# Kernel tuning notes

Measured on AMD Instinct MI355X. Metric: run time of the kernel, lower is better.

The kernel has to match this reference:

```python
import jax, jax.numpy as jnp
import numpy as np

F_DIM, H, O = 128, 256, 256
NQ, EQ = 64, 512
ND, ED = 50000, 600000

PARAM_SHAPES = [
    ("qW1", (F_DIM, H)), ("qb1", (H,)), ("qW2", (H, H)), ("qb2", (H,)),
    ("qW3", (H, H)),     ("qb3", (H,)), ("qW4", (H, O)), ("qb4", (O,)),
    ("dW1", (F_DIM, H)), ("db1", (H,)), ("dW2", (H, H)), ("db2", (H,)),
    ("dW3", (H, H)),     ("db3", (H,)), ("dW4", (H, O)), ("db4", (O,)),
    ("lW1", (2 * O, O)), ("lb1", (O,)),
    ("lW2", (O, O // 2)), ("lb2", (O // 2,)),
    ("lW3", (O // 2, 8)), ("lb3", (8,)),
]

def setup_inputs() -> dict:
    key = jax.random.key(0)
    ks = jax.random.split(key, 4 + len(PARAM_SHAPES))
    inp = {
        "query_in_feat": jax.random.normal(ks[0], (NQ, F_DIM), jnp.float32),
        "data_in_feat": jax.random.normal(ks[1], (ND, F_DIM), jnp.float32),
        "query_edge_list": jax.random.randint(ks[2], (2, EQ), 0, NQ),
        "data_edge_list": jax.random.randint(ks[3], (2, ED), 0, ND),
    }
    for i, (name, shape) in enumerate(PARAM_SHAPES):
        fan_in = shape[0] if len(shape) == 2 else 1
        inp[name] = jax.random.normal(ks[4 + i], shape, jnp.float32) * (1.0 / np.sqrt(fan_in))
    return inp

def _mlp2(x, W1, b1, W2, b2):
    return jnp.maximum(x @ W1 + b1, 0.0) @ W2 + b2

def _gin_conv(x, src, dst, W1, b1, W2, b2):
    # GINConv (eps=0): MLP(x_i + sum_{j->i} x_j); gather x[src], scatter-add at dst
    agg = jax.ops.segment_sum(x[src], dst, num_segments=x.shape[0])
    return _mlp2(x + agg, W1, b1, W2, b2)

def _gin(x, edge_index, p):
    src, dst = edge_index[0], edge_index[1]
    h = jnp.maximum(_gin_conv(x, src, dst, *p[:4]), 0.0)  # ReLU between convs
    return _gin_conv(h, src, dst, *p[4:])

def reference(query_in_feat, data_in_feat, query_edge_list, data_edge_list,
              qW1, qb1, qW2, qb2, qW3, qb3, qW4, qb4,
              dW1, db1, dW2, db2, dW3, db3, dW4, db4,
              lW1, lb1, lW2, lb2, lW3, lb3):
    qx = _gin(query_in_feat, query_edge_list, (qW1, qb1, qW2, qb2, qW3, qb3, qW4, qb4))
    dx = _gin(data_in_feat, data_edge_list, (dW1, db1, dW2, db2, dW3, db3, dW4, db4))
    # global_add_pool with batch = zeros -> single-graph sum
    qp = jnp.sum(qx, axis=0, keepdims=True)  # [1, O]
    dp = jnp.sum(dx, axis=0, keepdims=True)  # [1, O]
    h = jnp.concatenate([qp, dp], axis=1)    # [1, 2*O]
    h = jnp.maximum(h @ lW1 + lb1, 0.0)
    h = jnp.maximum(h @ lW2 + lb2, 0.0)
    h = jnp.maximum(h @ lW3 + lb3, 0.0)
    return h.reshape(1, 8)
```

## Files before the change

### kernel.cpp

```cpp
#include <hip/hip_runtime.h>
#include <hip/hip_bf16.h>


#define NQ 64
#define EQ 512
#define ND 50000
#define ED 600000
#define FDIM 128
#define HDIM 256

typedef __attribute__((ext_vector_type(8))) short short8;
typedef __attribute__((ext_vector_type(4))) float f32x4;
typedef __attribute__((ext_vector_type(2))) float floatx2;
typedef __attribute__((ext_vector_type(4))) unsigned short us4;
typedef __attribute__((ext_vector_type(2))) unsigned short us2;

__device__ __forceinline__ unsigned short f2bf(float f) {
    union { float f; unsigned u; } v; v.f = f;
    unsigned r = v.u + 0x7FFF + ((v.u >> 16) & 1);
    return (unsigned short)(r >> 16);
}
__device__ __forceinline__ float bf2f(unsigned short u) {
    union { unsigned u; float f; } v; v.u = ((unsigned)u) << 16;
    return v.f;
}


struct PackDesc {
    const float* W[8];
    unsigned short* Wp[8];
    int KT[8];
    int start[9];
};

__device__ __forceinline__ void pack_unit(const PackDesc& pd, int unit, int l) {
    int m = 0;
    while (m < 7 && unit >= pd.start[m + 1]) ++m;
    const int local = unit - pd.start[m];
    const int KT = pd.KT[m];
    const int kt = local % KT;
    const int ct = local / KT;
    const float* W = pd.W[m];
    unsigned short* Wp = pd.Wp[m];
    const int row = kt * 32 + (l >> 4) * 8;
    const int col = ct * 16 + (l & 15);
    short8 v;
#pragma unroll
    for (int j = 0; j < 8; ++j) v[j] = (short)f2bf(W[(size_t)(row + j) * 256 + col]);
    *(short8*)(Wp + (((size_t)(ct * KT + kt)) * 64 + l) * 8) = v;
}


__global__ void prepass(const float* __restrict__ xd, const float* __restrict__ xq,
                        unsigned short* __restrict__ bx, long long nd4, long long n4,
                        int cvt_b, PackDesc pd, int pack_units, int pack_b,
                        const int* __restrict__ d_dst, int* __restrict__ d_deg,
                        const int* __restrict__ q_dst, int* __restrict__ q_deg,
                        int d_eb) {
    const int b = blockIdx.x;
    const int tid = threadIdx.x;
    if (b < cvt_b) {
        long long i = (long long)b * 256 + tid;
        if (i >= n4) return;
        const float* src = (i < nd4) ? (xd + i * 4) : (xq + (i - nd4) * 4);
        float4 v = *(const float4*)src;
        us4 o;
        o[0] = f2bf(v.x); o[1] = f2bf(v.y); o[2] = f2bf(v.z); o[3] = f2bf(v.w);
        *(us4*)(bx + i * 4) = o;
    } else if (b < cvt_b + pack_b) {
        const int unit = (b - cvt_b) * 4 + (tid >> 6);
        if (unit < pack_units) pack_unit(pd, unit, tid & 63);
    } else {
        const int cb = b - cvt_b - pack_b;
        if (cb < d_eb) {
            int e = cb * 256 + tid;
            if (e < ED) atomicAdd(&d_deg[d_dst[e]], 1);
        } else {
            int e = (cb - d_eb) * 256 + tid;
            if (e < EQ) atomicAdd(&q_deg[q_dst[e]], 1);
        }
    }
}


__device__ __forceinline__ void scan1_body(const int* deg, int* rowptr, int* bsum,
                                           int n, int blk) {
    __shared__ int sh[256];
    const int t = threadIdx.x;
    const int i = blk * 256 + t;
    const int v = (i < n) ? deg[i] : 0;
    sh[t] = v;
    __syncthreads();
    for (int off = 1; off < 256; off <<= 1) {
        int x = (t >= off) ? sh[t - off] : 0;
        __syncthreads();
        sh[t] += x;
        __syncthreads();
    }
    if (i < n) rowptr[i] = sh[t] - v;
    if (t == 255) bsum[blk] = sh[255];
}

__global__ void scan_phase1_both(const int* __restrict__ d_deg, int* __restrict__ d_rowptr,
                                 int* __restrict__ d_bsum,
                                 const int* __restrict__ q_deg, int* __restrict__ q_rowptr,
                                 int* __restrict__ q_bsum, int dblocks) {
    int b = blockIdx.x;
    if (b < dblocks) scan1_body(d_deg, d_rowptr, d_bsum, ND, b);
    else             scan1_body(q_deg, q_rowptr, q_bsum, NQ, b - dblocks);
}

__device__ __forceinline__ void scan2_body(const int* bsum, int* boff, int* rowptr_n, int nb) {
    __shared__ int sh[256];
    const int t = threadIdx.x;
    const int v = (t < nb) ? bsum[t] : 0;
    sh[t] = v;
    __syncthreads();
    for (int off = 1; off < 256; off <<= 1) {
        int x = (t >= off) ? sh[t - off] : 0;
        __syncthreads();
        sh[t] += x;
        __syncthreads();
    }
    if (t < nb) boff[t] = sh[t] - v;
    if (t == 255) *rowptr_n = sh[255];
}

__global__ void scan_phase2_both(const int* __restrict__ d_bsum, int* __restrict__ d_boff,
                                 int* __restrict__ d_rowptr_n, int d_nb,
                                 const int* __restrict__ q_bsum, int* __restrict__ q_boff,
                                 int* __restrict__ q_rowptr_n, int q_nb) {
    if (blockIdx.x == 0) scan2_body(d_bsum, d_boff, d_rowptr_n, d_nb);
    else                 scan2_body(q_bsum, q_boff, q_rowptr_n, q_nb);
}

__global__ void scan_phase3_both(int* __restrict__ d_rowptr, const int* __restrict__ d_boff,
                                 int* __restrict__ d_cursor,
                                 int* __restrict__ q_rowptr, const int* __restrict__ q_boff,
                                 int* __restrict__ q_cursor, int dblocks) {
    int b = blockIdx.x;
    if (b < dblocks) {
        int i = b * 256 + threadIdx.x;
        if (i < ND) {
            int r = d_rowptr[i] + d_boff[b];
            d_rowptr[i] = r; d_cursor[i] = r;
        }
    } else {
        int i = (b - dblocks) * 256 + threadIdx.x;
        if (i < NQ) {
            int r = q_rowptr[i] + q_boff[b - dblocks];
            q_rowptr[i] = r; q_cursor[i] = r;
        }
    }
}

__global__ void fill_csr_both(const int* __restrict__ d_src, const int* __restrict__ d_dst,
                              int* __restrict__ d_cursor, int* __restrict__ d_csrsrc,
                              const int* __restrict__ q_src, const int* __restrict__ q_dst,
                              int* __restrict__ q_cursor, int* __restrict__ q_csrsrc,
                              int dblocks) {
    int b = blockIdx.x;
    if (b < dblocks) {
        int e = b * 256 + threadIdx.x;
        if (e < ED) {
            int p = atomicAdd(&d_cursor[d_dst[e]], 1);
            d_csrsrc[p] = d_src[e];
        }
    } else {
        int e = (b - dblocks) * 256 + threadIdx.x;
        if (e < EQ) {
            int p = atomicAdd(&q_cursor[q_dst[e]], 1);
            q_csrsrc[p] = q_src[e];
        }
    }
}


template <int F>
__global__ void gin_agg_dual(const unsigned short* __restrict__ xd, const int* __restrict__ rpd,
                             const int* __restrict__ csd, unsigned short* __restrict__ od,
                             const unsigned short* __restrict__ xq, const int* __restrict__ rpq,
                             const int* __restrict__ csq, unsigned short* __restrict__ oq) {
    constexpr int V = F / 64;
    const unsigned short* x; const int* rowptr; const int* csr; unsigned short* out; int node;
    if ((int)blockIdx.x < ND) { x = xd; rowptr = rpd; csr = csd; out = od; node = blockIdx.x; }
    else { x = xq; rowptr = rpq; csr = csq; out = oq; node = blockIdx.x - ND; }

    const int t = threadIdx.x;
    const int beg = rowptr[node];
    const int end = rowptr[node + 1];

    float acc[V];
    {
        const unsigned short* p = x + (size_t)node * F + t * V;
        if constexpr (V == 4) {
            us4 v = *(const us4*)p;
#pragma unroll
            for (int i = 0; i < 4; ++i) acc[i] = bf2f(v[i]);
        } else {
            us2 v = *(const us2*)p;
            acc[0] = bf2f(v[0]); acc[1] = bf2f(v[1]);
        }
    }
    int j = beg;
    for (; j + 1 < end; j += 2) {
        const unsigned short* p0 = x + (size_t)csr[j] * F + t * V;
        const unsigned short* p1 = x + (size_t)csr[j + 1] * F + t * V;
        if constexpr (V == 4) {
            us4 v0 = *(const us4*)p0;
            us4 v1 = *(const us4*)p1;
#pragma unroll
            for (int i = 0; i < 4; ++i) acc[i] += bf2f(v0[i]) + bf2f(v1[i]);
        } else {
            us2 v0 = *(const us2*)p0;
            us2 v1 = *(const us2*)p1;
            acc[0] += bf2f(v0[0]) + bf2f(v1[0]);
            acc[1] += bf2f(v0[1]) + bf2f(v1[1]);
        }
    }
    if (j < end) {
        const unsigned short* p0 = x + (size_t)csr[j] * F + t * V;
        if constexpr (V == 4) {
            us4 v0 = *(const us4*)p0;
#pragma unroll
            for (int i = 0; i < 4; ++i) acc[i] += bf2f(v0[i]);
        } else {
            us2 v0 = *(const us2*)p0;
            acc[0] += bf2f(v0[0]); acc[1] += bf2f(v0[1]);
        }
    }
    unsigned short* po = out + (size_t)node * F + t * V;
    if constexpr (V == 4) {
        us4 r;
#pragma unroll
        for (int i = 0; i < 4; ++i) r[i] = f2bf(acc[i]);
        *(us4*)po = r;
    } else {
        us2 r; r[0] = f2bf(acc[0]); r[1] = f2bf(acc[1]);
        *(us2*)po = r;
    }
}


__global__ void gin_agg_f8_256_dual(const unsigned char* __restrict__ xd,
                                    const int* __restrict__ rpd, const int* __restrict__ csd,
                                    unsigned short* __restrict__ od,
                                    const unsigned char* __restrict__ xq,
                                    const int* __restrict__ rpq, const int* __restrict__ csq,
                                    unsigned short* __restrict__ oq) {
    const unsigned char* x; const int* rowptr; const int* csr; unsigned short* out; int node;
    if ((int)blockIdx.x < ND) { x = xd; rowptr = rpd; csr = csd; out = od; node = blockIdx.x; }
    else { x = xq; rowptr = rpq; csr = csq; out = oq; node = blockIdx.x - ND; }

    const int t = threadIdx.x;
    const int beg = rowptr[node];
    const int end = rowptr[node + 1];

    float a0, a1, a2, a3;
    {
        const unsigned w = *(const unsigned*)(x + (size_t)node * 256 + t * 4);
        floatx2 lo = __builtin_amdgcn_cvt_pk_f32_fp8((int)w, false);
        floatx2 hi = __builtin_amdgcn_cvt_pk_f32_fp8((int)w, true);
        a0 = lo[0]; a1 = lo[1]; a2 = hi[0]; a3 = hi[1];
    }
    int j = beg;
    for (; j + 1 < end; j += 2) {
        const unsigned w0 = *(const unsigned*)(x + (size_t)csr[j] * 256 + t * 4);
        const unsigned w1 = *(const unsigned*)(x + (size_t)csr[j + 1] * 256 + t * 4);
        floatx2 l0 = __builtin_amdgcn_cvt_pk_f32_fp8((int)w0, false);
        floatx2 h0 = __builtin_amdgcn_cvt_pk_f32_fp8((int)w0, true);
        floatx2 l1 = __builtin_amdgcn_cvt_pk_f32_fp8((int)w1, false);
        floatx2 h1 = __builtin_amdgcn_cvt_pk_f32_fp8((int)w1, true);
        a0 += l0[0] + l1[0]; a1 += l0[1] + l1[1];
        a2 += h0[0] + h1[0]; a3 += h0[1] + h1[1];
    }
    if (j < end) {
        const unsigned w0 = *(const unsigned*)(x + (size_t)csr[j] * 256 + t * 4);
        floatx2 l0 = __builtin_amdgcn_cvt_pk_f32_fp8((int)w0, false);
        floatx2 h0 = __builtin_amdgcn_cvt_pk_f32_fp8((int)w0, true);
        a0 += l0[0]; a1 += l0[1]; a2 += h0[0]; a3 += h0[1];
    }
    us4 r;
    r[0] = f2bf(a0); r[1] = f2bf(a1); r[2] = f2bf(a2); r[3] = f2bf(a3);
    *(us4*)(out + (size_t)node * 256 + t * 4) = r;
}


template <int KIN>
__global__ __launch_bounds__(256) void mlp_dual(
    const unsigned short* __restrict__ Ad,
    const unsigned short* __restrict__ W1pd, const float* __restrict__ b1d,
    const unsigned short* __restrict__ W2pd, const float* __restrict__ b2d,
    unsigned char* __restrict__ C8d, int ndb,
    const unsigned short* __restrict__ Aq,
    const unsigned short* __restrict__ W1pq, const float* __restrict__ b1q,
    const unsigned short* __restrict__ W2pq, const float* __restrict__ b2q,
    unsigned char* __restrict__ C8q) {
    constexpr int KT1 = KIN / 32;
    __shared__ __align__(16) unsigned short lds[64 * 256];

    const unsigned short* A; const unsigned short* W1p; const float* b1;
    const unsigned short* W2p; const float* b2;
    unsigned char* C8; int row0, N;
    if ((int)blockIdx.x < ndb) {
        A = Ad; W1p = W1pd; b1 = b1d; W2p = W2pd; b2 = b2d;
        C8 = C8d; row0 = blockIdx.x * 64; N = ND;
    } else {
        A = Aq; W1p = W1pq; b1 = b1q; W2p = W2pq; b2 = b2q;
        C8 = C8q; row0 = 0; N = NQ;
    }

    const int tid = threadIdx.x;
    const int lane = tid & 63;
    const int wv = tid >> 6;
    const int lrow = lane & 15;
    const int lk2 = (lane >> 4) * 8;
    const int nrows = (N - row0 < 64) ? (N - row0) : 64;

    for (int idx = tid; idx < nrows * (KIN / 8); idx += 256) {
        const int r = idx / (KIN / 8);
        const int k8 = (idx % (KIN / 8)) * 8;
        short8 v = *(const short8*)(A + (size_t)(row0 + r) * KIN + k8);
        unsigned byte = (unsigned)((r * KIN + k8) * 2) ^ (unsigned)((r & 7) << 4);
        *(short8*)((char*)lds + byte) = v;
    }
    __syncthreads();

    f32x4 acc1[4][4];
#pragma unroll
    for (int fm = 0; fm < 4; ++fm)
#pragma unroll
        for (int fn = 0; fn < 4; ++fn) acc1[fm][fn] = (f32x4)(0.f);

    const unsigned short* W1Base = W1p + ((size_t)(wv * 4) * KT1 * 64 + lane) * 8;
    for (int kt = 0; kt < KT1; ++kt) {
        short8 a[4], bf[4];
#pragma unroll
        for (int fm = 0; fm < 4; ++fm) {
            const int r = fm * 16 + lrow;
            unsigned byte = (unsigned)((r * KIN + kt * 32 + lk2) * 2) ^ (unsigned)((r & 7) << 4);
            a[fm] = *(const short8*)((const char*)lds + byte);
        }
#pragma unroll
        for (int fn = 0; fn < 4; ++fn)
            bf[fn] = *(const short8*)(W1Base + ((size_t)fn * KT1 + kt) * 64 * 8);
#pragma unroll
        for (int fm = 0; fm < 4; ++fm)
#pragma unroll
            for (int fn = 0; fn < 4; ++fn)
                acc1[fm][fn] = __builtin_amdgcn_mfma_f32_16x16x32_bf16(
                    a[fm], bf[fn], acc1[fm][fn], 0, 0, 0);
    }
    __syncthreads();

#pragma unroll
    for (int fn = 0; fn < 4; ++fn) {
        const int col = wv * 64 + fn * 16 + lrow;
        const float bv = b1[col];
#pragma unroll
        for (int fm = 0; fm < 4; ++fm) {
            const int rbase = fm * 16 + (lane >> 4) * 4;
#pragma unroll
            for (int r = 0; r < 4; ++r) {
                const int row = rbase + r;
                const float v = fmaxf(acc1[fm][fn][r] + bv, 0.f);
                unsigned byte = (unsigned)((row * 256 + col) * 2) ^ (unsigned)((row & 7) << 4);
                *(unsigned short*)((char*)lds + byte) = f2bf(v);
            }
        }
    }
    __syncthreads();

    f32x4 acc2[4][4];
#pragma unroll
    for (int fm = 0; fm < 4; ++fm)
#pragma unroll
        for (int fn = 0; fn < 4; ++fn) acc2[fm][fn] = (f32x4)(0.f);

    const unsigned short* W2Base = W2p + ((size_t)(wv * 4) * 8 * 64 + lane) * 8;
    for (int kt = 0; kt < 8; ++kt) {
        short8 a[4], bf[4];
#pragma unroll
        for (int fm = 0; fm < 4; ++fm) {
            const int r = fm * 16 + lrow;
            unsigned byte = (unsigned)((r * 256 + kt * 32 + lk2) * 2) ^ (unsigned)((r & 7) << 4);
            a[fm] = *(const short8*)((const char*)lds + byte);
        }
#pragma unroll
        for (int fn = 0; fn < 4; ++fn)
            bf[fn] = *(const short8*)(W2Base + ((size_t)fn * 8 + kt) * 64 * 8);
#pragma unroll
        for (int fm = 0; fm < 4; ++fm)
#pragma unroll
            for (int fn = 0; fn < 4; ++fn)
                acc2[fm][fn] = __builtin_amdgcn_mfma_f32_16x16x32_bf16(
                    a[fm], bf[fn], acc2[fm][fn], 0, 0, 0);
    }

#pragma unroll
    for (int fn = 0; fn < 4; ++fn) {
        const int col = wv * 64 + fn * 16 + lrow;
        const float bv = b2[col];
#pragma unroll
        for (int fm = 0; fm < 4; ++fm) {
            const int rbase = row0 + fm * 16 + (lane >> 4) * 4;
#pragma unroll
            for (int r = 0; r < 4; ++r) {
                const int row = rbase + r;
                if (row < N) {
                    float v = fmaxf(acc2[fm][fn][r] + bv, 0.f);
                    unsigned p = (unsigned)__builtin_amdgcn_cvt_pk_fp8_f32(v, v, 0, false);
                    C8[(size_t)row * 256 + col] = (unsigned char)(p & 0xff);
                }
            }
        }
    }
}


__global__ __launch_bounds__(256) void t1pool_dual(
    const unsigned short* __restrict__ Ad,
    const unsigned short* __restrict__ W1pd, const float* __restrict__ b1d,
    float* __restrict__ poold, int ndb,
    const unsigned short* __restrict__ Aq,
    const unsigned short* __restrict__ W1pq, const float* __restrict__ b1q,
    float* __restrict__ poolq) {
    const unsigned short* A; const unsigned short* W1p; const float* b1;
    float* pool; int row0, N;
    if ((int)blockIdx.x < ndb) {
        A = Ad; W1p = W1pd; b1 = b1d; pool = poold; row0 = blockIdx.x * 64; N = ND;
    } else {
        A = Aq; W1p = W1pq; b1 = b1q; pool = poolq; row0 = 0; N = NQ;
    }

    const int tid = threadIdx.x;
    const int lane = tid & 63;
    const int wv = tid >> 6;
    const int lrow = lane & 15;
    const int lk2 = (lane >> 4) * 8;

    f32x4 acc[4][4];
#pragma unroll
    for (int fm = 0; fm < 4; ++fm)
#pragma unroll
        for (int fn = 0; fn < 4; ++fn) acc[fm][fn] = (f32x4)(0.f);

    const unsigned short* W1Base = W1p + ((size_t)(wv * 4) * 8 * 64 + lane) * 8;
    const unsigned short* Alane = A + (size_t)(row0 + lrow) * 256 + lk2;

#pragma unroll
    for (int kt = 0; kt < 8; ++kt) {
        short8 a[4], bf[4];
#pragma unroll
        for (int fm = 0; fm < 4; ++fm)
            a[fm] = *(const short8*)(Alane + (size_t)(fm * 16) * 256 + kt * 32);
#pragma unroll
        for (int fn = 0; fn < 4; ++fn)
            bf[fn] = *(const short8*)(W1Base + ((size_t)fn * 8 + kt) * 64 * 8);
#pragma unroll
        for (int fm = 0; fm < 4; ++fm)
#pragma unroll
            for (int fn = 0; fn < 4; ++fn)
                acc[fm][fn] = __builtin_amdgcn_mfma_f32_16x16x32_bf16(
                    a[fm], bf[fn], acc[fm][fn], 0, 0, 0);
    }

#pragma unroll
    for (int fn = 0; fn < 4; ++fn) {
        const int col = wv * 64 + fn * 16 + lrow;
        const float bv = b1[col];
        float ps = 0.f;
#pragma unroll
        for (int fm = 0; fm < 4; ++fm) {
            const int rbase = row0 + fm * 16 + (lane >> 4) * 4;
#pragma unroll
            for (int r = 0; r < 4; ++r) {
                const int row = rbase + r;
                if (row < N) ps += fmaxf(acc[fm][fn][r] + bv, 0.f);
            }
        }
        ps += __shfl_xor(ps, 16);
        ps += __shfl_xor(ps, 32);
        if ((lane >> 4) == 0) atomicAdd(&pool[col], ps);
    }
}


__global__ void mlp_head(const float* __restrict__ poolT1,
                         const float* __restrict__ qW4, const float* __restrict__ qb4,
                         const float* __restrict__ dW4, const float* __restrict__ db4,
                         const float* __restrict__ lW1, const float* __restrict__ lb1,
                         const float* __restrict__ lW2, const float* __restrict__ lb2,
                         const float* __restrict__ lW3, const float* __restrict__ lb3,
                         float* __restrict__ out) {
    __shared__ float h0[512];
    __shared__ float h1[256];
    __shared__ float h2[128];
    const int t = threadIdx.x;

    float accq = (float)NQ * qb4[t];
    float accd = (float)ND * db4[t];
    for (int k = 0; k < 256; ++k) {
        accq += poolT1[k] * qW4[(size_t)k * 256 + t];
        accd += poolT1[256 + k] * dW4[(size_t)k * 256 + t];
    }
    h0[t] = accq;
    h0[t + 256] = accd;
    __syncthreads();

    float acc = lb1[t];
    for (int k = 0; k < 512; ++k) acc += h0[k] * lW1[k * 256 + t];
    h1[t] = fmaxf(acc, 0.f);
    __syncthreads();

    if (t < 128) {
        float a = lb2[t];
        for (int k = 0; k < 256; ++k) a += h1[k] * lW2[k * 128 + t];
        h2[t] = fmaxf(a, 0.f);
    }
    __syncthreads();

    if (t < 8) {
        float a = lb3[t];
        for (int k = 0; k < 128; ++k) a += h2[k] * lW3[k * 8 + t];
        out[t] = fmaxf(a, 0.f);
    }
}


extern "C" void kernel_launch(void* const* d_in, const int* in_sizes, int n_in,
                              void* d_out, int out_size, void* d_ws, size_t ws_size,
                              hipStream_t stream) {
    const float* q_x  = (const float*)d_in[0];
    const float* d_x  = (const float*)d_in[1];
    const int*   q_el = (const int*)d_in[2];
    const int*   d_el = (const int*)d_in[3];
    const float* qW1 = (const float*)d_in[4];  const float* qb1 = (const float*)d_in[5];
    const float* qW2 = (const float*)d_in[6];  const float* qb2 = (const float*)d_in[7];
    const float* qW3 = (const float*)d_in[8];  const float* qb3 = (const float*)d_in[9];
    const float* qW4 = (const float*)d_in[10]; const float* qb4 = (const float*)d_in[11];
    const float* dW1 = (const float*)d_in[12]; const float* db1 = (const float*)d_in[13];
    const float* dW2 = (const float*)d_in[14]; const float* db2 = (const float*)d_in[15];
    const float* dW3 = (const float*)d_in[16]; const float* db3 = (const float*)d_in[17];
    const float* dW4 = (const float*)d_in[18]; const float* db4 = (const float*)d_in[19];
    const float* lW1 = (const float*)d_in[20]; const float* lb1 = (const float*)d_in[21];
    const float* lW2 = (const float*)d_in[22]; const float* lb2 = (const float*)d_in[23];
    const float* lW3 = (const float*)d_in[24]; const float* lb3 = (const float*)d_in[25];
    (void)in_sizes; (void)n_in; (void)out_size; (void)ws_size;

    const int* q_src = q_el;  const int* q_dst = q_el + EQ;
    const int* d_src = d_el;  const int* d_dst = d_el + ED;

    char* wsb = (char*)d_ws;
    size_t off = 0;
    auto alloc = [&](size_t bytes) { void* p = wsb + off; off += (bytes + 255) & ~(size_t)255; return p; };

    unsigned short* bxd = (unsigned short*)alloc((size_t)ND * FDIM * 2);
    unsigned short* bxq = (unsigned short*)alloc((size_t)NQ * FDIM * 2);
    unsigned short* dag = (unsigned short*)alloc((size_t)ND * FDIM * 2);
    unsigned short* qag = (unsigned short*)alloc((size_t)NQ * FDIM * 2);
    unsigned char*  h8d = (unsigned char*)alloc((size_t)ND * HDIM);
    unsigned char*  h8q = (unsigned char*)alloc((size_t)NQ * HDIM);
    unsigned short* had = (unsigned short*)alloc((size_t)ND * HDIM * 2);
    unsigned short* haq = (unsigned short*)alloc((size_t)(NQ + 64) * HDIM * 2);
    float* poolT1 = (float*)alloc(512 * 4);
    int* d_deg    = (int*)alloc((size_t)ND * 4);
    int* q_deg    = (int*)alloc((size_t)NQ * 4);
    int* d_rowptr = (int*)alloc((size_t)(ND + 1) * 4);
    int* d_cursor = (int*)alloc((size_t)ND * 4);
    int* d_csrsrc = (int*)alloc((size_t)ED * 4);
    int* d_bsum   = (int*)alloc(256 * 4);
    int* d_boff   = (int*)alloc(256 * 4);
    int* q_rowptr = (int*)alloc((size_t)(NQ + 1) * 4);
    int* q_cursor = (int*)alloc((size_t)NQ * 4);
    int* q_csrsrc = (int*)alloc((size_t)EQ * 4);
    int* q_bsum   = (int*)alloc(256 * 4);
    int* q_boff   = (int*)alloc(256 * 4);
    unsigned short* pdW1 = (unsigned short*)alloc((size_t)FDIM * 256 * 2);
    unsigned short* pdW2 = (unsigned short*)alloc((size_t)HDIM * 256 * 2);
    unsigned short* pdW3 = (unsigned short*)alloc((size_t)HDIM * 256 * 2);
    unsigned short* pqW1 = (unsigned short*)alloc((size_t)FDIM * 256 * 2);
    unsigned short* pqW2 = (unsigned short*)alloc((size_t)HDIM * 256 * 2);
    unsigned short* pqW3 = (unsigned short*)alloc((size_t)HDIM * 256 * 2);

    hipMemsetAsync(poolT1, 0, 512 * 4, stream);
    hipMemsetAsync(d_deg, 0, (char*)(q_deg + NQ) - (char*)d_deg, stream);

    const int d_eb = (ED + 255) / 256;
    const int q_eb = (EQ + 255) / 256;
    const int d_nb = (ND + 255) / 256;
    const int q_nb = (NQ + 255) / 256;
    {
        PackDesc pd;
        const float* Ws[6] = {dW1, dW2, dW3, qW1, qW2, qW3};
        unsigned short* Wps[6] = {pdW1, pdW2, pdW3, pqW1, pqW2, pqW3};
        int kts[6] = {4, 8, 8, 4, 8, 8};
        int s = 0;
        for (int i = 0; i < 6; ++i) {
            pd.W[i] = Ws[i]; pd.Wp[i] = Wps[i]; pd.KT[i] = kts[i];
            pd.start[i] = s; s += 16 * kts[i];
        }
        for (int i = 6; i < 8; ++i) { pd.W[i] = dW1; pd.Wp[i] = pdW1; pd.KT[i] = 4; pd.start[i] = s; }
        pd.start[8] = s;
        const int pack_units = s;
        const int pack_b = (s + 3) / 4;
        long long nd4 = (long long)ND * FDIM / 4;
        long long n4 = nd4 + (long long)NQ * FDIM / 4;
        const int cvt_b = (int)((n4 + 255) / 256);
        prepass<<<cvt_b + pack_b + d_eb + q_eb, 256, 0, stream>>>(
            d_x, q_x, bxd, nd4, n4, cvt_b, pd, pack_units, pack_b,
            d_dst, d_deg, q_dst, q_deg, d_eb);
    }

    scan_phase1_both<<<d_nb + q_nb, 256, 0, stream>>>(d_deg, d_rowptr, d_bsum,
                                                      q_deg, q_rowptr, q_bsum, d_nb);
    scan_phase2_both<<<2, 256, 0, stream>>>(d_bsum, d_boff, d_rowptr + ND, d_nb,
                                            q_bsum, q_boff, q_rowptr + NQ, q_nb);
    scan_phase3_both<<<d_nb + q_nb, 256, 0, stream>>>(d_rowptr, d_boff, d_cursor,
                                                      q_rowptr, q_boff, q_cursor, d_nb);
    fill_csr_both<<<d_eb + q_eb, 256, 0, stream>>>(d_src, d_dst, d_cursor, d_csrsrc,
                                                   q_src, q_dst, q_cursor, q_csrsrc, d_eb);

    const int ndb = (ND + 63) / 64;

    gin_agg_dual<FDIM><<<ND + NQ, 64, 0, stream>>>(bxd, d_rowptr, d_csrsrc, dag,
                                                   bxq, q_rowptr, q_csrsrc, qag);
    mlp_dual<FDIM><<<ndb + 1, 256, 0, stream>>>(
        dag, pdW1, db1, pdW2, db2, h8d, ndb,
        qag, pqW1, qb1, pqW2, qb2, h8q);

    gin_agg_f8_256_dual<<<ND + NQ, 64, 0, stream>>>(
        h8d, d_rowptr, d_csrsrc, had, h8q, q_rowptr, q_csrsrc, haq);
    t1pool_dual<<<ndb + 1, 256, 0, stream>>>(
        had, pdW3, db3, poolT1 + 256, ndb,
        haq, pqW3, qb3, poolT1);

    mlp_head<<<1, 256, 0, stream>>>(poolT1, qW4, qb4, dW4, db4,
                                    lW1, lb1, lW2, lb2, lW3, lb3, (float*)d_out);
}
```

Before: 245.0 us.

## Store input features as fp8, pack two nodes per block, split MLP head

Input features are now converted to fp8 instead of bf16 in the prepass. The first aggregation uses a new fp8 gather kernel where each 64-thread block handles two nodes with 32 lanes each, which halves gather bytes and block count. The single-block serial MLP head becomes four kernels that split the K dimension across blocks and combine partial sums with atomics. The memsets are merged into one. The change trades input precision for bandwidth, and the head now pays extra launches and atomic contention in exchange for parallelism.

```diff
diff --git a/kernel.cpp b/kernel.cpp
--- a/kernel.cpp
+++ b/kernel.cpp
@@ -52,7 +52,7 @@
 
 
 __global__ void prepass(const float* __restrict__ xd, const float* __restrict__ xq,
-                        unsigned short* __restrict__ bx, long long nd4, long long n4,
+                        unsigned char* __restrict__ x8, long long nd4, long long n4,
                         int cvt_b, PackDesc pd, int pack_units, int pack_b,
                         const int* __restrict__ d_dst, int* __restrict__ d_deg,
                         const int* __restrict__ q_dst, int* __restrict__ q_deg,
@@ -64,9 +64,9 @@
         if (i >= n4) return;
         const float* src = (i < nd4) ? (xd + i * 4) : (xq + (i - nd4) * 4);
         float4 v = *(const float4*)src;
-        us4 o;
-        o[0] = f2bf(v.x); o[1] = f2bf(v.y); o[2] = f2bf(v.z); o[3] = f2bf(v.w);
-        *(us4*)(bx + i * 4) = o;
+        int p = __builtin_amdgcn_cvt_pk_fp8_f32(v.x, v.y, 0, false);
+        p = __builtin_amdgcn_cvt_pk_fp8_f32(v.z, v.w, p, true);
+        *(unsigned*)(x8 + i * 4) = (unsigned)p;
     } else if (b < cvt_b + pack_b) {
         const int unit = (b - cvt_b) * 4 + (tid >> 6);
         if (unit < pack_units) pack_unit(pd, unit, tid & 63);
@@ -176,69 +176,39 @@
 }
 
 
-template <int F>
-__global__ void gin_agg_dual(const unsigned short* __restrict__ xd, const int* __restrict__ rpd,
-                             const int* __restrict__ csd, unsigned short* __restrict__ od,
-                             const unsigned short* __restrict__ xq, const int* __restrict__ rpq,
-                             const int* __restrict__ csq, unsigned short* __restrict__ oq) {
-    constexpr int V = F / 64;
-    const unsigned short* x; const int* rowptr; const int* csr; unsigned short* out; int node;
-    if ((int)blockIdx.x < ND) { x = xd; rowptr = rpd; csr = csd; out = od; node = blockIdx.x; }
-    else { x = xq; rowptr = rpq; csr = csq; out = oq; node = blockIdx.x - ND; }
-
-    const int t = threadIdx.x;
+__global__ void gin_agg_f8_128_dual(const unsigned char* __restrict__ xd,
+                                    const int* __restrict__ rpd, const int* __restrict__ csd,
+                                    unsigned short* __restrict__ od,
+                                    const unsigned char* __restrict__ xq,
+                                    const int* __restrict__ rpq, const int* __restrict__ csq,
+                                    unsigned short* __restrict__ oq, int ndpair) {
+    const unsigned char* x; const int* rowptr; const int* csr; unsigned short* out; int nb;
+    if ((int)blockIdx.x < ndpair) { x = xd; rowptr = rpd; csr = csd; out = od; nb = blockIdx.x; }
+    else { x = xq; rowptr = rpq; csr = csq; out = oq; nb = blockIdx.x - ndpair; }
+
+    const int t = threadIdx.x;
+    const int node = nb * 2 + (t >> 5);
+    const int c = t & 31;
+
     const int beg = rowptr[node];
     const int end = rowptr[node + 1];
 
-    float acc[V];
+    float a0, a1, a2, a3;
     {
-        const unsigned short* p = x + (size_t)node * F + t * V;
-        if constexpr (V == 4) {
-            us4 v = *(const us4*)p;
-#pragma unroll
-            for (int i = 0; i < 4; ++i) acc[i] = bf2f(v[i]);
-        } else {
-            us2 v = *(const us2*)p;
-            acc[0] = bf2f(v[0]); acc[1] = bf2f(v[1]);
-        }
-    }
-    int j = beg;
-    for (; j + 1 < end; j += 2) {
-        const unsigned short* p0 = x + (size_t)csr[j] * F + t * V;
-        const unsigned short* p1 = x + (size_t)csr[j + 1] * F + t * V;
-        if constexpr (V == 4) {
-            us4 v0 = *(const us4*)p0;
-            us4 v1 = *(const us4*)p1;
-#pragma unroll
-            for (int i = 0; i < 4; ++i) acc[i] += bf2f(v0[i]) + bf2f(v1[i]);
-        } else {
-            us2 v0 = *(const us2*)p0;
-            us2 v1 = *(const us2*)p1;
-            acc[0] += bf2f(v0[0]) + bf2f(v1[0]);
-            acc[1] += bf2f(v0[1]) + bf2f(v1[1]);
-        }
-    }
-    if (j < end) {
-        const unsigned short* p0 = x + (size_t)csr[j] * F + t * V;
-        if constexpr (V == 4) {
-            us4 v0 = *(const us4*)p0;
-#pragma unroll
-            for (int i = 0; i < 4; ++i) acc[i] += bf2f(v0[i]);
-        } else {
-            us2 v0 = *(const us2*)p0;
-            acc[0] += bf2f(v0[0]); acc[1] += bf2f(v0[1]);
-        }
-    }
-    unsigned short* po = out + (size_t)node * F + t * V;
-    if constexpr (V == 4) {
-        us4 r;
-#pragma unroll
-        for (int i = 0; i < 4; ++i) r[i] = f2bf(acc[i]);
-        *(us4*)po = r;
-    } else {
-        us2 r; r[0] = f2bf(acc[0]); r[1] = f2bf(acc[1]);
-        *(us2*)po = r;
-    }
+        const unsigned w = *(const unsigned*)(x + (size_t)node * 128 + c * 4);
+        floatx2 lo = __builtin_amdgcn_cvt_pk_f32_fp8((int)w, false);
+        floatx2 hi = __builtin_amdgcn_cvt_pk_f32_fp8((int)w, true);
+        a0 = lo[0]; a1 = lo[1]; a2 = hi[0]; a3 = hi[1];
+    }
+    for (int j = beg; j < end; ++j) {
+        const unsigned w = *(const unsigned*)(x + (size_t)csr[j] * 128 + c * 4);
+        floatx2 lo = __builtin_amdgcn_cvt_pk_f32_fp8((int)w, false);
+        floatx2 hi = __builtin_amdgcn_cvt_pk_f32_fp8((int)w, true);
+        a0 += lo[0]; a1 += lo[1]; a2 += hi[0]; a3 += hi[1];
+    }
+    us4 r;
+    r[0] = f2bf(a0); r[1] = f2bf(a1); r[2] = f2bf(a2); r[3] = f2bf(a3);
+    *(us4*)(out + (size_t)node * 128 + c * 4) = r;
 }
 
 
@@ -485,45 +455,49 @@
     }
 }
 
-
-__global__ void mlp_head(const float* __restrict__ poolT1,
-                         const float* __restrict__ qW4, const float* __restrict__ qb4,
-                         const float* __restrict__ dW4, const float* __restrict__ db4,
-                         const float* __restrict__ lW1, const float* __restrict__ lb1,
-                         const float* __restrict__ lW2, const float* __restrict__ lb2,
-                         const float* __restrict__ lW3, const float* __restrict__ lb3,
-                         float* __restrict__ out) {
-    __shared__ float h0[512];
-    __shared__ float h1[256];
-    __shared__ float h2[128];
-    const int t = threadIdx.x;
-
-    float accq = (float)NQ * qb4[t];
-    float accd = (float)ND * db4[t];
-    for (int k = 0; k < 256; ++k) {
-        accq += poolT1[k] * qW4[(size_t)k * 256 + t];
-        accd += poolT1[256 + k] * dW4[(size_t)k * 256 + t];
-    }
-    h0[t] = accq;
-    h0[t + 256] = accd;
-    __syncthreads();
-
-    float acc = lb1[t];
-    for (int k = 0; k < 512; ++k) acc += h0[k] * lW1[k * 256 + t];
-    h1[t] = fmaxf(acc, 0.f);
-    __syncthreads();
-
-    if (t < 128) {
-        float a = lb2[t];
-        for (int k = 0; k < 256; ++k) a += h1[k] * lW2[k * 128 + t];
-        h2[t] = fmaxf(a, 0.f);
-    }
-    __syncthreads();
-
+__global__ void head_w4(const float* __restrict__ poolT1,
+                        const float* __restrict__ qW4, const float* __restrict__ qb4,
+                        const float* __restrict__ dW4, const float* __restrict__ db4,
+                        float* __restrict__ s0) {
+    const int b = blockIdx.x;
+    const int m = b >> 3;
+    const int ks = (b & 7) * 32;
+    const int t = threadIdx.x;
+    const float* W = m ? dW4 : qW4;
+    const float* P = poolT1 + (m ? 256 : 0);
+    float acc = 0.f;
+    for (int k = ks; k < ks + 32; ++k) acc += P[k] * W[(size_t)k * 256 + t];
+    if ((b & 7) == 0) acc += m ? (float)ND * db4[t] : (float)NQ * qb4[t];
+    atomicAdd(&s0[m * 256 + t], acc);
+}
+
+__global__ void head_l1(const float* __restrict__ s0, const float* __restrict__ lW1,
+                        const float* __restrict__ lb1, float* __restrict__ s1) {
+    const int ks = blockIdx.x * 32;
+    const int t = threadIdx.x;
+    float acc = 0.f;
+    for (int k = ks; k < ks + 32; ++k) acc += s0[k] * lW1[(size_t)k * 256 + t];
+    if (blockIdx.x == 0) acc += lb1[t];
+    atomicAdd(&s1[t], acc);
+}
+
+__global__ void head_l2(const float* __restrict__ s1, const float* __restrict__ lW2,
+                        const float* __restrict__ lb2, float* __restrict__ s2) {
+    const int ks = blockIdx.x * 32;
+    const int t = threadIdx.x;
+    float acc = 0.f;
+    for (int k = ks; k < ks + 32; ++k) acc += fmaxf(s1[k], 0.f) * lW2[(size_t)k * 128 + t];
+    if (blockIdx.x == 0) acc += lb2[t];
+    atomicAdd(&s2[t], acc);
+}
+
+__global__ void head_l3(const float* __restrict__ s2, const float* __restrict__ lW3,
+                        const float* __restrict__ lb3, float* __restrict__ out) {
+    const int t = threadIdx.x;
     if (t < 8) {
-        float a = lb3[t];
-        for (int k = 0; k < 128; ++k) a += h2[k] * lW3[k * 8 + t];
-        out[t] = fmaxf(a, 0.f);
+        float acc = lb3[t];
+        for (int k = 0; k < 128; ++k) acc += fmaxf(s2[k], 0.f) * lW3[k * 8 + t];
+        out[t] = fmaxf(acc, 0.f);
     }
 }
 
@@ -555,8 +529,8 @@
     size_t off = 0;
     auto alloc = [&](size_t bytes) { void* p = wsb + off; off += (bytes + 255) & ~(size_t)255; return p; };
 
-    unsigned short* bxd = (unsigned short*)alloc((size_t)ND * FDIM * 2);
-    unsigned short* bxq = (unsigned short*)alloc((size_t)NQ * FDIM * 2);
+    unsigned char*  x8d = (unsigned char*)alloc((size_t)ND * FDIM);
+    unsigned char*  x8q = (unsigned char*)alloc((size_t)NQ * FDIM);
     unsigned short* dag = (unsigned short*)alloc((size_t)ND * FDIM * 2);
     unsigned short* qag = (unsigned short*)alloc((size_t)NQ * FDIM * 2);
     unsigned char*  h8d = (unsigned char*)alloc((size_t)ND * HDIM);
@@ -564,8 +538,12 @@
     unsigned short* had = (unsigned short*)alloc((size_t)ND * HDIM * 2);
     unsigned short* haq = (unsigned short*)alloc((size_t)(NQ + 64) * HDIM * 2);
     float* poolT1 = (float*)alloc(512 * 4);
+    float* s0     = (float*)alloc(512 * 4);
+    float* s1     = (float*)alloc(256 * 4);
+    float* s2     = (float*)alloc(128 * 4);
     int* d_deg    = (int*)alloc((size_t)ND * 4);
     int* q_deg    = (int*)alloc((size_t)NQ * 4);
+    char* zero_end = wsb + off;
     int* d_rowptr = (int*)alloc((size_t)(ND + 1) * 4);
     int* d_cursor = (int*)alloc((size_t)ND * 4);
     int* d_csrsrc = (int*)alloc((size_t)ED * 4);
@@ -583,8 +561,7 @@
     unsigned short* pqW2 = (unsigned short*)alloc((size_t)HDIM * 256 * 2);
     unsigned short* pqW3 = (unsigned short*)alloc((size_t)HDIM * 256 * 2);
 
-    hipMemsetAsync(poolT1, 0, 512 * 4, stream);
-    hipMemsetAsync(d_deg, 0, (char*)(q_deg + NQ) - (char*)d_deg, stream);
+    hipMemsetAsync(poolT1, 0, (size_t)(zero_end - (char*)poolT1), stream);
 
     const int d_eb = (ED + 255) / 256;
     const int q_eb = (EQ + 255) / 256;
@@ -608,7 +585,7 @@
         long long n4 = nd4 + (long long)NQ * FDIM / 4;
         const int cvt_b = (int)((n4 + 255) / 256);
         prepass<<<cvt_b + pack_b + d_eb + q_eb, 256, 0, stream>>>(
-            d_x, q_x, bxd, nd4, n4, cvt_b, pd, pack_units, pack_b,
+            d_x, q_x, x8d, nd4, n4, cvt_b, pd, pack_units, pack_b,
             d_dst, d_deg, q_dst, q_deg, d_eb);
     }
 
@@ -621,10 +598,12 @@
     fill_csr_both<<<d_eb + q_eb, 256, 0, stream>>>(d_src, d_dst, d_cursor, d_csrsrc,
                                                    q_src, q_dst, q_cursor, q_csrsrc, d_eb);
 
+    const int ndpair = ND / 2;
+    const int qpair = NQ / 2;
     const int ndb = (ND + 63) / 64;
 
-    gin_agg_dual<FDIM><<<ND + NQ, 64, 0, stream>>>(bxd, d_rowptr, d_csrsrc, dag,
-                                                   bxq, q_rowptr, q_csrsrc, qag);
+    gin_agg_f8_128_dual<<<ndpair + qpair, 64, 0, stream>>>(
+        x8d, d_rowptr, d_csrsrc, dag, x8q, q_rowptr, q_csrsrc, qag, ndpair);
     mlp_dual<FDIM><<<ndb + 1, 256, 0, stream>>>(
         dag, pdW1, db1, pdW2, db2, h8d, ndb,
         qag, pqW1, qb1, pqW2, qb2, h8q);
@@ -635,6 +614,8 @@
         had, pdW3, db3, poolT1 + 256, ndb,
         haq, pqW3, qb3, poolT1);
 
-    mlp_head<<<1, 256, 0, stream>>>(poolT1, qW4, qb4, dW4, db4,
-                                    lW1, lb1, lW2, lb2, lW3, lb3, (float*)d_out);
-}
+    head_w4<<<16, 256, 0, stream>>>(poolT1, qW4, qb4, dW4, db4, s0);
+    head_l1<<<16, 256, 0, stream>>>(s0, lW1, lb1, s1);
+    head_l2<<<8, 128, 0, stream>>>(s1, lW2, lb2, s2);
+    head_l3<<<1, 64, 0, stream>>>(s2, lW3, lb3, (float*)d_out);
+}
```

After: 227.5 us. 1.08x faster.
